# Performance work log

Measured on AMD Instinct MI355X. Metric: run time of the kernel, lower is better.

Reference implementation:

```python
import jax, jax.numpy as jnp
import numpy as np

N = 220500          # samples (5 s @ 44.1 kHz)
C = 28              # gammatone channels
L_GT = 1000         # gammatone FIR length (source default)
L_ENV = 2000        # envelope FIR length (source default)
START2POLE = 5      # Start2PoleHP -> HP applied to channels 4: (24 channels)
NGAMMA = 4          # cascaded gammatone passes
RECOMB_DB = 10.0    # Recombination_dB
EQUIV0DBSPL = 100.0 # CONFIG.equiv0dBSPL
AHR = 0.0           # CONFIG.ahr


def fir_grouped(x, h):
    """Causal per-channel FIR: y[c,n] = sum_k h[c,k] x[c,n-k]. x:[C,N], h:[C,L]."""
    L = h.shape[1]
    y = jax.lax.conv_general_dilated(
        x[None], h[:, None, ::-1], (1,), [(L - 1, 0)],
        feature_group_count=x.shape[0],
        dimension_numbers=("NCH", "OIH", "NCH"))
    return y[0]


def fir1(x, h):
    return fir_grouped(x[None, :], h[None, :])[0]


def setup_inputs() -> dict:
    key = jax.random.key(0)
    ks = jax.random.split(key, 10)
    dec_gt = jnp.exp(-jnp.arange(L_GT, dtype=jnp.float32) / 80.0)
    dec_env = jnp.exp(-jnp.arange(L_ENV, dtype=jnp.float32) / 300.0)
    x = jax.random.normal(ks[0], (N,), dtype=jnp.float32)
    gtn_imp = jax.random.normal(ks[1], (C, L_GT), dtype=jnp.float32) * 0.05 * dec_gt[None]
    hp_imp = jax.random.normal(ks[2], (C - START2POLE + 1, L_GT), dtype=jnp.float32) * 0.05 * dec_gt[None]
    chan_lpf_imp = (0.01 + 0.002 * jax.random.normal(ks[3], (C, L_ENV), dtype=jnp.float32)) * dec_env[None]
    delta256 = jnp.zeros((256,), jnp.float32).at[0].set(1.0)
    src_fwd = delta256 + 0.01 * jax.random.normal(ks[4], (256,), dtype=jnp.float32)
    src_bwd = delta256 + 0.01 * jax.random.normal(ks[5], (256,), dtype=jnp.float32)
    lpf = jnp.zeros((133,), jnp.float32).at[0].set(1.0) + 0.01 * jax.random.normal(ks[6], (133,), dtype=jnp.float32)
    expansion_ratios = 1.0 + jax.random.uniform(ks[7], (C,), dtype=jnp.float32)
    eq_loud_db = 100.0 + 10.0 * jax.random.uniform(ks[8], (C,), dtype=jnp.float32)
    delays = jax.random.randint(ks[9], (C,), 0, 200, dtype=jnp.int32)
    return {"x": x, "src_fwd": src_fwd, "src_bwd": src_bwd, "lpf": lpf,
            "gtn_imp": gtn_imp, "hp_imp": hp_imp, "chan_lpf_imp": chan_lpf_imp,
            "expansion_ratios": expansion_ratios, "eq_loud_db": eq_loud_db,
            "delays": delays}


def _cochlea(x, gtn_imp, hp_imp, chan_lpf_imp, delays, expansion_ratios, eq_loud_db, equiv_0dB_SPL):
    n = x.shape[0]
    c = gtn_imp.shape[0]
    # gammatone filterbank: NGAMMA cascaded grouped causal FIRs
    pass_n = jnp.broadcast_to(x[None, :], (c, n))
    for _ in range(NGAMMA):
        pass_n = fir_grouped(pass_n, gtn_imp)
    # per-channel delay compensation (shift left by dly, zero-fill tail)
    idx = jnp.arange(n, dtype=jnp.int32)[None, :] + delays[:, None]  # [C,N]
    gathered = jnp.take_along_axis(pass_n, jnp.minimum(idx, n - 1), axis=1)
    pass_del = jnp.where(idx < n, gathered, 0.0)
    # high-pass correction on channels Start2PoleHP-1:
    s = START2POLE - 1
    pass_del = pass_del.at[s:].set(fir_grouped(pass_del[s:], hp_imp))
    # envelope: forward-backward low-pass of rectified signal
    env_f = fir_grouped(jnp.abs(pass_del), chan_lpf_imp)
    env = fir_grouped(jnp.abs(env_f[:, ::-1]), chan_lpf_imp)[:, ::-1]
    # loudness recruitment
    envlp_max = (10.0 ** (0.05 * (eq_loud_db - equiv_0dB_SPL)))[:, None]
    env_cl = jnp.minimum(jnp.clip(env, 1e-9, None), envlp_max)
    env_norm = jnp.clip(env_cl / envlp_max, 1e-6, None)
    gain = env_norm ** (jnp.clip(expansion_ratios, -5.0, None)[:, None] - 1.0)
    gain = jnp.minimum(gain, 100.0)
    coch = pass_del * gain
    power = 10.0 ** (-0.05 * RECOMB_DB)
    return coch.sum(axis=0) * power


def reference(x, src_fwd, src_bwd, lpf, gtn_imp, hp_imp, chan_lpf_imp,
              expansion_ratios, eq_loud_db, delays):
    # level bookkeeping (as in HearingLoss.forward)
    levelreFS = 10.0 * jnp.log10(jnp.mean(x ** 2))  # noqa: F841 (calibration only)
    equiv_0dB_SPL = EQUIV0DBSPL + AHR
    # free-field -> cochlea correction
    xc = fir1(x, src_fwd)
    coch = _cochlea(xc, gtn_imp, hp_imp, chan_lpf_imp, delays,
                    expansion_ratios, eq_loud_db, equiv_0dB_SPL)
    # cochlea -> free-field correction, then 18 kHz anti-alias LPF
    out = fir1(fir1(coch, src_bwd), lpf)
    return out
```

## Files before the change

### kernel.cpp

```cpp
#include <hip/hip_runtime.h>
#include <math.h>

#define NSAMP 220500
#define NCH   28
#define HPCH  24
#define TILE  2048
#define BLOCK 256

#define LP_GT4 4032
#define LP_HP  1008
#define LP_ENV 2016
#define LP_SRC 288
#define LP_LPF 144

#define NC_GT 126
#define NC_HP 33
#define NC_EF 64
#define NC_EB 63

typedef __attribute__((ext_vector_type(4))) float f32x4;
typedef __attribute__((ext_vector_type(8))) short bf16x8;

__device__ __forceinline__ int phys9(int u) { return u + (u >> 3); }

__device__ __forceinline__ unsigned short f2bf(float x) {
    unsigned u = __float_as_uint(x);
    u += 0x7FFFu + ((u >> 16) & 1u);
    return (unsigned short)(u >> 16);
}

#define MFMA32 __builtin_amdgcn_mfma_f32_16x16x32_bf16

__global__ void prep_frag(const float* __restrict__ taps, int pitch,
                          unsigned short* __restrict__ TF, int NC,
                          int isAsc, int split, long planeStride)
{
    const int s  = blockIdx.x;
    const int ch = blockIdx.y;
    const int l  = threadIdx.x;
    const int m  = l & 15, hib = (l >> 4) * 8;
    unsigned short* dst = TF + ((size_t)ch * NC + s) * 512 + l * 8;
#pragma unroll
    for (int i = 0; i < 8; i++) {
        int kap = hib + i;
        int k = isAsc ? (32 * s + kap - m) : (32 * s + m - 1 - kap);
        float val = (k >= 0 && k < pitch) ? taps[(size_t)ch * pitch + k] : 0.f;
        unsigned short hh = f2bf(val);
        dst[i] = hh;
        if (split) {
            float fh = __uint_as_float((unsigned)hh << 16);
            dst[planeStride + i] = f2bf(val - fh);
        }
    }
}

template<int NC, bool ASC, bool SPLIT, bool ABSIN, bool DELAYED, bool GAIN>
__global__ __launch_bounds__(BLOCK)
void fir_mfma_pc(const float* __restrict__ in, long instride,
                 const unsigned short* __restrict__ TF, long planeStride,
                 float* __restrict__ out,
                 const int* __restrict__ delays, int chan0,
                 const float* __restrict__ ratios,
                 const float* __restrict__ eqloud)
{
    extern __shared__ float S[];
    unsigned short* sw = (unsigned short*)S;
    const int c  = blockIdx.y;
    const int jb = blockIdx.x * 4096;
    const float* __restrict__ xin = in + (long)c * instride;
    constexpr int E = 4112 + 32 * (NC - 1);
    const int o = ASC ? jb : (jb + 1 - 32 * (NC - 1));
    int d = 0;
    if (DELAYED) d = delays[chan0 + c];

    for (int e = threadIdx.x; e < E; e += BLOCK) {
        int p = o + e;
        float v = 0.f;
        if (DELAYED) { if (p >= 0 && p + d < NSAMP) v = xin[p + d]; }
        else         { if (p >= 0 && p < NSAMP)     v = xin[p]; }
        if (ABSIN) v = fabsf(v);
        sw[2 * phys9(e >> 1) + (e & 1)] = f2bf(v);
    }
    __syncthreads();

    const int lane = threadIdx.x & 63;
    const int w    = threadIdx.x >> 6;
    const int n    = lane & 15;
    const int hi   = lane >> 4;
    int vp = phys9(8 * n + 4 * hi + 512 * w + (ASC ? 0 : 16 * (NC - 1)));
    constexpr int DSTEP = ASC ? 18 : -18;

    const unsigned short* tp = TF + (size_t)c * NC * 512 + lane * 8;

    f32x4 ac0 = {0,0,0,0}, ac1 = {0,0,0,0}, ac2 = {0,0,0,0}, ac3 = {0,0,0,0};
    bf16x8 Ah = *(const bf16x8*)tp;
    bf16x8 Al = Ah;
    if (SPLIT) Al = *(const bf16x8*)(tp + planeStride);

#pragma unroll 1
    for (int s = 0; s < NC; ++s) {
        bf16x8 Nh = Ah, Nl = Al;
        if (s + 1 < NC) {
            Nh = *(const bf16x8*)(tp + (size_t)(s + 1) * 512);
            if (SPLIT) Nl = *(const bf16x8*)(tp + planeStride + (size_t)(s + 1) * 512);
        }
        const float* sp = S + vp;
        union U { float f[4]; bf16x8 v; };
        U b0, b1, b2, b3;
        b0.f[0]=sp[0];   b0.f[1]=sp[1];   b0.f[2]=sp[2];   b0.f[3]=sp[3];
        b1.f[0]=sp[144]; b1.f[1]=sp[145]; b1.f[2]=sp[146]; b1.f[3]=sp[147];
        b2.f[0]=sp[288]; b2.f[1]=sp[289]; b2.f[2]=sp[290]; b2.f[3]=sp[291];
        b3.f[0]=sp[432]; b3.f[1]=sp[433]; b3.f[2]=sp[434]; b3.f[3]=sp[435];
        ac0 = MFMA32(Ah, b0.v, ac0, 0, 0, 0);
        ac1 = MFMA32(Ah, b1.v, ac1, 0, 0, 0);
        ac2 = MFMA32(Ah, b2.v, ac2, 0, 0, 0);
        ac3 = MFMA32(Ah, b3.v, ac3, 0, 0, 0);
        if (SPLIT) {
            ac0 = MFMA32(Al, b0.v, ac0, 0, 0, 0);
            ac1 = MFMA32(Al, b1.v, ac1, 0, 0, 0);
            ac2 = MFMA32(Al, b2.v, ac2, 0, 0, 0);
            ac3 = MFMA32(Al, b3.v, ac3, 0, 0, 0);
        }
        Ah = Nh;
        if (SPLIT) Al = Nl;
        vp += DSTEP;
    }

    float* __restrict__ yo = out + (long)c * NSAMP;
    const int j0 = jb + 1024 * w + 16 * n + 4 * hi;

    if (!GAIN) {
        if (j0 < NSAMP)       *(f32x4*)(yo + j0)       = ac0;
        if (j0 + 256 < NSAMP) *(f32x4*)(yo + j0 + 256) = ac1;
        if (j0 + 512 < NSAMP) *(f32x4*)(yo + j0 + 512) = ac2;
        if (j0 + 768 < NSAMP) *(f32x4*)(yo + j0 + 768) = ac3;
    } else {
        const float emax = exp10f(0.05f * (eqloud[c] - 100.0f));
        const float er   = fmaxf(ratios[c], -5.0f) - 1.0f;
#define GAINST(ACC, OFS) { int j = j0 + (OFS); if (j < NSAMP) {            \
            f32x4 pv = *(f32x4*)(yo + j);                                   \
            _Pragma("unroll")                                               \
            for (int r = 0; r < 4; r++) {                                   \
                float env = ACC[r];                                         \
                float ecl = fminf(fmaxf(env, 1e-9f), emax);                 \
                float enr = fmaxf(ecl / emax, 1e-6f);                       \
                float g   = fminf(powf(enr, er), 100.0f);                   \
                pv[r] *= g;                                                 \
            }                                                               \
            *(f32x4*)(yo + j) = pv; } }
        GAINST(ac0, 0) GAINST(ac1, 256) GAINST(ac2, 512) GAINST(ac3, 768)
#undef GAINST
    }
}

static inline size_t lds_pc(int NC)
{
    int E = 4112 + 32 * (NC - 1);
    int D = (E + 1) / 2;
    return (size_t)(D + (D >> 3) + 8) * 4;
}

template<bool ASC>
__device__ __forceinline__ void group8r(const float (&LO)[8], const float (&HI)[8],
                                        float (&acc)[8], const f32x4 (&T)[2])
{
#pragma unroll
    for (int kp = 0; kp < 8; kp++) {
        const float hk = T[kp >> 2][kp & 3];
#pragma unroll
        for (int j = 0; j < 8; j++) {
            const int m = ASC ? (j + kp) : (8 + j - kp);
            const float w = (m < 8) ? LO[m] : HI[m - 8];
            acc[j] = fmaf(hk, w, acc[j]);
        }
    }
}

template<int Lpad, bool DELAYED>
__global__ __launch_bounds__(BLOCK)
void fir_blk(const float* __restrict__ in, long instride,
             const float* __restrict__ taps, int tapstride,
             float* __restrict__ out, long ostride,
             const int* __restrict__ delays, int chan0)
{
    extern __shared__ float s[];
    const int c  = blockIdx.y;
    const int n0 = blockIdx.x * TILE;
    const float* __restrict__ xin = in + (long)c * instride;
    float* __restrict__ y         = out + (long)c * ostride;
    int d = 0;
    if (DELAYED) d = delays[chan0 + c];

    constexpr int E = TILE + Lpad - 1;
    for (int i = threadIdx.x; i < E; i += BLOCK) {
        int p = n0 - (Lpad - 1) + i;
        float v = 0.f;
        if (p >= 0 && p < NSAMP) {
            int q = p + d;
            if (!DELAYED || q < NSAMP) v = xin[q];
        }
        s[phys9(i + 9)] = v;
    }
    __syncthreads();

    const int t = threadIdx.x;
    constexpr int LB = Lpad / 8;
    const int B = 9 * (t + LB);
    const f32x4* tv = (const f32x4*)(taps + (long)c * tapstride);

    float Ab[8], Bb[8], Cb[8];
    float acc[8] = {0,0,0,0,0,0,0,0};
#pragma unroll
    for (int m = 0; m < 8; m++) Ab[m] = s[B + m];
#pragma unroll
    for (int m = 0; m < 8; m++) Bb[m] = s[B + 9 + m];
    f32x4 TA[2], TB[2];
    TA[0] = tv[0]; TA[1] = tv[1];

    int Mb = B - 54;
    constexpr int NIT6 = Lpad / 48;
#pragma unroll 1
    for (int im = 0; im < NIT6; ++im) {
        const float* p = s + Mb;
#pragma unroll
        for (int m = 0; m < 8; m++) Cb[m] = p[45 + m];
        TB[0] = tv[2];  TB[1] = tv[3];
        group8r<false>(Ab, Bb, acc, TA);
#pragma unroll
        for (int m = 0; m < 8; m++) Bb[m] = p[36 + m];
        TA[0] = tv[4];  TA[1] = tv[5];
        group8r<false>(Cb, Ab, acc, TB);
#pragma unroll
        for (int m = 0; m < 8; m++) Ab[m] = p[27 + m];
        TB[0] = tv[6];  TB[1] = tv[7];
        group8r<false>(Bb, Cb, acc, TA);
#pragma unroll
        for (int m = 0; m < 8; m++) Cb[m] = p[18 + m];
        TA[0] = tv[8];  TA[1] = tv[9];
        group8r<false>(Ab, Bb, acc, TB);
#pragma unroll
        for (int m = 0; m < 8; m++) Bb[m] = p[9 + m];
        TB[0] = tv[10]; TB[1] = tv[11];
        group8r<false>(Cb, Ab, acc, TA);
#pragma unroll
        for (int m = 0; m < 8; m++) Ab[m] = p[0 + m];
        TA[0] = tv[12]; TA[1] = tv[13];
        group8r<false>(Bb, Cb, acc, TB);
        Mb -= 54;
        tv += 12;
    }

    const int nb = n0 + 8 * t;
#pragma unroll
    for (int j = 0; j < 8; j++)
        if (nb + j < NSAMP) y[nb + j] = acc[j];
}

static inline size_t lds_blk(int Lpad)
{
    int umax = TILE + Lpad + 8;
    return (size_t)(umax + (umax >> 3) + 16) * 4;
}

__global__ void conv_self(const float* __restrict__ a, int astride, int La,
                          float* __restrict__ out, int ostride, int Mlen, int Mpad)
{
    extern __shared__ float s[];
    const int c = blockIdx.y;
    const float* __restrict__ ar = a + (long)c * astride;
    for (int i = threadIdx.x; i < La; i += blockDim.x) s[i] = ar[i];
    __syncthreads();
    int m = blockIdx.x * blockDim.x + threadIdx.x;
    float acc = 0.f;
    for (int k = 0; k < La; k++) {
        int mi = m - k;
        float bv = ((unsigned)mi < (unsigned)La) ? s[mi] : 0.f;
        acc = fmaf(s[k], bv, acc);
    }
    if (m < Mpad) out[(long)c * ostride + m] = (m < Mlen) ? acc : 0.f;
}

__global__ void pad_copy(const float* __restrict__ src, int L, int sstride,
                         float* __restrict__ dst, int Lpad)
{
    int c = blockIdx.y;
    int k = blockIdx.x * blockDim.x + threadIdx.x;
    if (k < Lpad) dst[(long)c * Lpad + k] = (k < L) ? src[(long)c * sstride + k] : 0.f;
}

__global__ void delay_copy(const float* __restrict__ a, float* __restrict__ b,
                           const int* __restrict__ delays)
{
    int c = blockIdx.y;
    int n = blockIdx.x * blockDim.x + threadIdx.x;
    if (n < NSAMP) {
        int q = n + delays[c];
        b[(long)c * NSAMP + n] = (q < NSAMP) ? a[(long)c * NSAMP + q] : 0.f;
    }
}

__global__ void reduce_coch(const float* __restrict__ b, float* __restrict__ coch)
{
    int n = blockIdx.x * blockDim.x + threadIdx.x;
    if (n < NSAMP) {
        float sum = 0.f;
        for (int c = 0; c < NCH; c++) sum += b[(long)c * NSAMP + n];
        coch[n] = sum * 0.31622776601683794f;
    }
}

extern "C" void kernel_launch(void* const* d_in, const int* in_sizes, int n_in,
                              void* d_out, int out_size, void* d_ws, size_t ws_size,
                              hipStream_t stream)
{
    const float* x       = (const float*)d_in[0];
    const float* src_fwd = (const float*)d_in[1];
    const float* src_bwd = (const float*)d_in[2];
    const float* lpf     = (const float*)d_in[3];
    const float* gtn     = (const float*)d_in[4];
    const float* hp      = (const float*)d_in[5];
    const float* clpf    = (const float*)d_in[6];
    const float* ratios  = (const float*)d_in[7];
    const float* eqloud  = (const float*)d_in[8];
    const int*   delays  = (const int*)d_in[9];
    float* out = (float*)d_out;

    float* ws   = (float*)d_ws;
    const size_t CNs = (size_t)NCH * NSAMP;
    float* bufA  = ws;
    float* bufB  = bufA + CNs;
    float* xc    = bufB + CNs;
    float* coch  = xc + NSAMP;
    float* t1    = coch + NSAMP;
    float* h2    = t1 + NSAMP;
    float* h4    = h2 + (size_t)NCH * 2000;
    float* hpP   = h4 + (size_t)NCH * LP_GT4;
    float* clpfP = hpP + (size_t)HPCH * LP_HP;
    float* sfP   = clpfP + (size_t)NCH * LP_ENV;
    float* sbP   = sfP + LP_SRC;
    float* lpP   = sbP + LP_SRC;

    unsigned short* TFgt = (unsigned short*)(lpP + LP_LPF);
    const long gtPlane = (long)NCH * NC_GT * 512;
    unsigned short* TFhp = TFgt + 2 * gtPlane;
    unsigned short* TFef = TFhp + (size_t)HPCH * NC_HP * 512;
    unsigned short* TFeb = TFef + (size_t)NCH * NC_EF * 512;

    dim3 blk(BLOCK);
    const int NT  = (NSAMP + TILE - 1) / TILE;
    const int NB4 = (NSAMP + 4095) / 4096;

    conv_self<<<dim3(8, NCH), blk, 1000 * 4, stream>>>(
        gtn, 1000, 1000, h2, 2000, 1999, 1999);
    conv_self<<<dim3((LP_GT4 + BLOCK - 1) / BLOCK, NCH), blk, 1999 * 4, stream>>>(
        h2, 2000, 1999, h4, LP_GT4, 3997, LP_GT4);
    pad_copy<<<dim3(4, HPCH), blk, 0, stream>>>(hp, 1000, 1000, hpP, LP_HP);
    pad_copy<<<dim3(8, NCH), blk, 0, stream>>>(clpf, 2000, 2000, clpfP, LP_ENV);
    pad_copy<<<dim3(2, 1), blk, 0, stream>>>(src_fwd, 256, 256, sfP, LP_SRC);
    pad_copy<<<dim3(2, 1), blk, 0, stream>>>(src_bwd, 256, 256, sbP, LP_SRC);
    pad_copy<<<dim3(1, 1), blk, 0, stream>>>(lpf, 133, 133, lpP, LP_LPF);

    prep_frag<<<dim3(NC_GT, NCH), dim3(64), 0, stream>>>(
        h4, LP_GT4, TFgt, NC_GT, 0, 1, gtPlane);
    prep_frag<<<dim3(NC_HP, HPCH), dim3(64), 0, stream>>>(
        hpP, LP_HP, TFhp, NC_HP, 0, 0, 0);
    prep_frag<<<dim3(NC_EF, NCH), dim3(64), 0, stream>>>(
        clpfP, LP_ENV, TFef, NC_EF, 0, 0, 0);
    prep_frag<<<dim3(NC_EB, NCH), dim3(64), 0, stream>>>(
        clpfP, LP_ENV, TFeb, NC_EB, 1, 0, 0);

    fir_blk<LP_SRC, false><<<dim3(NT, 1), blk, lds_blk(LP_SRC), stream>>>(
        x, 0, sfP, LP_SRC, xc, 0, nullptr, 0);

    fir_mfma_pc<NC_GT, false, true, false, false, false>
        <<<dim3(NB4, NCH), blk, lds_pc(NC_GT), stream>>>(
        xc, 0, TFgt, gtPlane, bufA, nullptr, 0, nullptr, nullptr);

    delay_copy<<<dim3((NSAMP + BLOCK - 1) / BLOCK, 4), blk, 0, stream>>>(
        bufA, bufB, delays);

    fir_mfma_pc<NC_HP, false, false, false, true, false>
        <<<dim3(NB4, HPCH), blk, lds_pc(NC_HP), stream>>>(
        bufA + 4 * (size_t)NSAMP, NSAMP, TFhp, 0, bufB + 4 * (size_t)NSAMP,
        delays, 4, nullptr, nullptr);

    fir_mfma_pc<NC_EF, false, false, true, false, false>
        <<<dim3(NB4, NCH), blk, lds_pc(NC_EF), stream>>>(
        bufB, NSAMP, TFef, 0, bufA, nullptr, 0, nullptr, nullptr);

    fir_mfma_pc<NC_EB, true, false, true, false, true>
        <<<dim3(NB4, NCH), blk, lds_pc(NC_EB), stream>>>(
        bufA, NSAMP, TFeb, 0, bufB, nullptr, 0, ratios, eqloud);

    reduce_coch<<<dim3((NSAMP + BLOCK - 1) / BLOCK), blk, 0, stream>>>(bufB, coch);

    fir_blk<LP_SRC, false><<<dim3(NT, 1), blk, lds_blk(LP_SRC), stream>>>(
        coch, 0, sbP, LP_SRC, t1, 0, nullptr, 0);
    fir_blk<LP_LPF, false><<<dim3(NT, 1), blk, lds_blk(LP_LPF), stream>>>(
        t1, 0, lpP, LP_LPF, out, 0, nullptr, 0);
}
```

Before: 500.9 us.

## Fold source FIRs into gammatone/tail filters and switch to 32x32 MFMA kernels

The forward source FIR is pre-convolved into the quadrupled gammatone impulse response, and the backward source FIR is pre-convolved with the anti-alias LPF, which removes two full-length signal passes and their intermediate buffers. The gammatone pass now computes four channels per block so each LDS tile of the input is reused across channels. The HP and envelope FIRs move to a new kernel built on 32x32x16 bf16 MFMA with a different LDS padding scheme. The trade-offs are longer combined filters (more MFMA steps) and a larger accumulator register footprint per wave.

```diff
diff --git a/kernel.cpp b/kernel.cpp
--- a/kernel.cpp
+++ b/kernel.cpp
@@ -8,18 +8,21 @@
 #define BLOCK 256
 
 #define LP_GT4 4032
+#define L_H4F  4252
+#define LP_H4F 4288
 #define LP_HP  1008
 #define LP_ENV 2016
-#define LP_SRC 288
-#define LP_LPF 144
-
-#define NC_GT 126
-#define NC_HP 33
-#define NC_EF 64
-#define NC_EB 63
-
-typedef __attribute__((ext_vector_type(4))) float f32x4;
-typedef __attribute__((ext_vector_type(8))) short bf16x8;
+#define L_TB   388
+#define LP_TB  432
+
+#define NC_GT 134
+#define NC_HP 65
+#define NC_EF 128
+#define NC_EB 128
+
+typedef __attribute__((ext_vector_type(4)))  float f32x4;
+typedef __attribute__((ext_vector_type(16))) float f32x16;
+typedef __attribute__((ext_vector_type(8)))  short bf16x8;
 
 __device__ __forceinline__ int phys9(int u) { return u + (u >> 3); }
 
@@ -29,7 +32,8 @@
     return (unsigned short)(u >> 16);
 }
 
-#define MFMA32 __builtin_amdgcn_mfma_f32_16x16x32_bf16
+#define MFMA16 __builtin_amdgcn_mfma_f32_16x16x32_bf16
+#define MFMA32 __builtin_amdgcn_mfma_f32_32x32x16_bf16
 
 __global__ void prep_frag(const float* __restrict__ taps, int pitch,
                           unsigned short* __restrict__ TF, int NC,
@@ -54,110 +58,209 @@
     }
 }
 
-template<int NC, bool ASC, bool SPLIT, bool ABSIN, bool DELAYED, bool GAIN>
+__global__ void prep_frag32(const float* __restrict__ taps, int pitch,
+                            unsigned short* __restrict__ TF, int NC, int isAsc)
+{
+    const int s  = blockIdx.x;
+    const int ch = blockIdx.y;
+    const int l  = threadIdx.x;
+    const int m  = l & 31, kb = (l >> 5) * 8;
+    unsigned short* dst = TF + ((size_t)ch * NC + s) * 512 + l * 8;
+#pragma unroll
+    for (int i = 0; i < 8; i++) {
+        int kap = kb + i;
+        int k = isAsc ? (16 * s + kap - m) : (16 * s + m - 17 - kap);
+        float val = (k >= 0 && k < pitch) ? taps[(size_t)ch * pitch + k] : 0.f;
+        dst[i] = f2bf(val);
+    }
+}
+
 __global__ __launch_bounds__(BLOCK)
-void fir_mfma_pc(const float* __restrict__ in, long instride,
-                 const unsigned short* __restrict__ TF, long planeStride,
-                 float* __restrict__ out,
-                 const int* __restrict__ delays, int chan0,
-                 const float* __restrict__ ratios,
-                 const float* __restrict__ eqloud)
+void gt4_mfma4(const float* __restrict__ x, const unsigned short* __restrict__ TF,
+               long plane, float* __restrict__ out)
 {
     extern __shared__ float S[];
-    unsigned short* sw = (unsigned short*)S;
-    const int c  = blockIdx.y;
-    const int jb = blockIdx.x * 4096;
-    const float* __restrict__ xin = in + (long)c * instride;
-    constexpr int E = 4112 + 32 * (NC - 1);
-    const int o = ASC ? jb : (jb + 1 - 32 * (NC - 1));
-    int d = 0;
-    if (DELAYED) d = delays[chan0 + c];
-
-    for (int e = threadIdx.x; e < E; e += BLOCK) {
-        int p = o + e;
-        float v = 0.f;
-        if (DELAYED) { if (p >= 0 && p + d < NSAMP) v = xin[p + d]; }
-        else         { if (p >= 0 && p < NSAMP)     v = xin[p]; }
-        if (ABSIN) v = fabsf(v);
-        sw[2 * phys9(e >> 1) + (e & 1)] = f2bf(v);
+    unsigned* S32 = (unsigned*)S;
+    const int jb = blockIdx.x * 2048;
+    const int c0 = blockIdx.y * 4;
+    const int o  = jb - 4255;
+    const int DW = 3160;
+
+    for (int v = threadIdx.x; v < DW; v += BLOCK) {
+        int p0 = o + 2 * v, p1 = p0 + 1;
+        float a = (p0 >= 0 && p0 < NSAMP) ? x[p0] : 0.f;
+        float b = (p1 >= 0 && p1 < NSAMP) ? x[p1] : 0.f;
+        S32[v + (v >> 4)] = (unsigned)f2bf(a) | ((unsigned)f2bf(b) << 16);
     }
     __syncthreads();
 
     const int lane = threadIdx.x & 63;
     const int w    = threadIdx.x >> 6;
     const int n    = lane & 15;
-    const int hi   = lane >> 4;
-    int vp = phys9(8 * n + 4 * hi + 512 * w + (ASC ? 0 : 16 * (NC - 1)));
-    constexpr int DSTEP = ASC ? 18 : -18;
+    const int hib  = lane >> 4;
+    int v0 = 256 * w + 8 * n + 4 * hib + 16 * (NC_GT - 1);
+    int vp = v0 + (v0 >> 4);
+
+    const unsigned short* t0  = TF + lane * 8;
+    const unsigned short* tc0 = t0 + (size_t)(c0 + 0) * NC_GT * 512;
+    const unsigned short* tc1 = t0 + (size_t)(c0 + 1) * NC_GT * 512;
+    const unsigned short* tc2 = t0 + (size_t)(c0 + 2) * NC_GT * 512;
+    const unsigned short* tc3 = t0 + (size_t)(c0 + 3) * NC_GT * 512;
+
+    f32x4 a00={0,0,0,0}, a01={0,0,0,0}, a10={0,0,0,0}, a11={0,0,0,0};
+    f32x4 a20={0,0,0,0}, a21={0,0,0,0}, a30={0,0,0,0}, a31={0,0,0,0};
+
+    bf16x8 h0 = *(const bf16x8*)tc0, h1 = *(const bf16x8*)tc1;
+    bf16x8 h2 = *(const bf16x8*)tc2, h3 = *(const bf16x8*)tc3;
+    bf16x8 l0 = *(const bf16x8*)(tc0 + plane), l1 = *(const bf16x8*)(tc1 + plane);
+    bf16x8 l2 = *(const bf16x8*)(tc2 + plane), l3 = *(const bf16x8*)(tc3 + plane);
+
+#pragma unroll 1
+    for (int s = 0; s < NC_GT; ++s) {
+        int sn = (s + 1 < NC_GT) ? s + 1 : s;
+        size_t off = (size_t)sn * 512;
+        bf16x8 nh0 = *(const bf16x8*)(tc0 + off);
+        bf16x8 nh1 = *(const bf16x8*)(tc1 + off);
+        bf16x8 nh2 = *(const bf16x8*)(tc2 + off);
+        bf16x8 nh3 = *(const bf16x8*)(tc3 + off);
+        bf16x8 nl0 = *(const bf16x8*)(tc0 + plane + off);
+        bf16x8 nl1 = *(const bf16x8*)(tc1 + plane + off);
+        bf16x8 nl2 = *(const bf16x8*)(tc2 + plane + off);
+        bf16x8 nl3 = *(const bf16x8*)(tc3 + plane + off);
+
+        const float* sp = S + vp;
+        union U { float f[4]; bf16x8 v; } b0, b1;
+        b0.f[0]=sp[0];   b0.f[1]=sp[1];   b0.f[2]=sp[2];   b0.f[3]=sp[3];
+        b1.f[0]=sp[136]; b1.f[1]=sp[137]; b1.f[2]=sp[138]; b1.f[3]=sp[139];
+
+        a00 = MFMA16(h0, b0.v, a00,0,0,0);  a00 = MFMA16(l0, b0.v, a00,0,0,0);
+        a10 = MFMA16(h1, b0.v, a10,0,0,0);  a10 = MFMA16(l1, b0.v, a10,0,0,0);
+        a20 = MFMA16(h2, b0.v, a20,0,0,0);  a20 = MFMA16(l2, b0.v, a20,0,0,0);
+        a30 = MFMA16(h3, b0.v, a30,0,0,0);  a30 = MFMA16(l3, b0.v, a30,0,0,0);
+        a01 = MFMA16(h0, b1.v, a01,0,0,0);  a01 = MFMA16(l0, b1.v, a01,0,0,0);
+        a11 = MFMA16(h1, b1.v, a11,0,0,0);  a11 = MFMA16(l1, b1.v, a11,0,0,0);
+        a21 = MFMA16(h2, b1.v, a21,0,0,0);  a21 = MFMA16(l2, b1.v, a21,0,0,0);
+        a31 = MFMA16(h3, b1.v, a31,0,0,0);  a31 = MFMA16(l3, b1.v, a31,0,0,0);
+
+        h0=nh0; h1=nh1; h2=nh2; h3=nh3;
+        l0=nl0; l1=nl1; l2=nl2; l3=nl3;
+        vp -= 17;
+    }
+
+    const int j0 = jb + 512 * w + 16 * n + 4 * hib;
+    float* y0 = out + (size_t)(c0 + 0) * NSAMP;
+    float* y1 = out + (size_t)(c0 + 1) * NSAMP;
+    float* y2 = out + (size_t)(c0 + 2) * NSAMP;
+    float* y3 = out + (size_t)(c0 + 3) * NSAMP;
+    if (j0 < NSAMP) {
+        *(f32x4*)(y0 + j0) = a00; *(f32x4*)(y1 + j0) = a10;
+        *(f32x4*)(y2 + j0) = a20; *(f32x4*)(y3 + j0) = a30;
+    }
+    if (j0 + 256 < NSAMP) {
+        *(f32x4*)(y0 + j0 + 256) = a01; *(f32x4*)(y1 + j0 + 256) = a11;
+        *(f32x4*)(y2 + j0 + 256) = a21; *(f32x4*)(y3 + j0 + 256) = a31;
+    }
+}
+
+template<int NC, bool ASC, bool ABSIN, bool DELAYED, bool GAIN>
+__global__ __launch_bounds__(BLOCK)
+void fir32(const float* __restrict__ in, long instride,
+           const unsigned short* __restrict__ TF,
+           float* __restrict__ out,
+           const int* __restrict__ delays, int chan0,
+           const float* __restrict__ ratios, const float* __restrict__ eqloud)
+{
+    extern __shared__ float S[];
+    unsigned* S32 = (unsigned*)S;
+    const int c  = blockIdx.y;
+    const int jb = blockIdx.x * 4096;
+    const float* __restrict__ xin = in + (size_t)c * instride;
+    const int o = ASC ? jb : (jb + 17 - 16 * (NC - 1));
+    int d = 0;
+    if (DELAYED) d = delays[chan0 + c];
+
+    const int DW = 2040 + 8 * (NC - 1);
+    for (int v = threadIdx.x; v < DW; v += BLOCK) {
+        int p0 = o + 2 * v, p1 = p0 + 1;
+        float a = 0.f, b = 0.f;
+        if (DELAYED) {
+            if (p0 >= 0 && p0 + d < NSAMP) a = xin[p0 + d];
+            if (p1 >= 0 && p1 + d < NSAMP) b = xin[p1 + d];
+        } else {
+            if (p0 >= 0 && p0 < NSAMP) a = xin[p0];
+            if (p1 >= 0 && p1 < NSAMP) b = xin[p1];
+        }
+        if (ABSIN) { a = fabsf(a); b = fabsf(b); }
+        S32[v + (v >> 4)] = (unsigned)f2bf(a) | ((unsigned)f2bf(b) << 16);
+    }
+    __syncthreads();
+
+    const int lane = threadIdx.x & 63;
+    const int w    = threadIdx.x >> 6;
+    const int n    = lane & 31;
+    const int h5   = lane >> 5;
+    int v = 512 * w + 16 * n + 4 * h5 + (ASC ? 0 : 8 * (NC - 1));
 
     const unsigned short* tp = TF + (size_t)c * NC * 512 + lane * 8;
 
-    f32x4 ac0 = {0,0,0,0}, ac1 = {0,0,0,0}, ac2 = {0,0,0,0}, ac3 = {0,0,0,0};
-    bf16x8 Ah = *(const bf16x8*)tp;
-    bf16x8 Al = Ah;
-    if (SPLIT) Al = *(const bf16x8*)(tp + planeStride);
+    f32x16 acc;
+#pragma unroll
+    for (int i = 0; i < 16; ++i) acc[i] = 0.f;
+    bf16x8 A = *(const bf16x8*)tp;
 
 #pragma unroll 1
     for (int s = 0; s < NC; ++s) {
-        bf16x8 Nh = Ah, Nl = Al;
-        if (s + 1 < NC) {
-            Nh = *(const bf16x8*)(tp + (size_t)(s + 1) * 512);
-            if (SPLIT) Nl = *(const bf16x8*)(tp + planeStride + (size_t)(s + 1) * 512);
+        int sn = (s + 1 < NC) ? s + 1 : s;
+        bf16x8 An = *(const bf16x8*)(tp + (size_t)sn * 512);
+        int vp = v + (v >> 4);
+        const float* sp = S + vp;
+        union U { float f[4]; bf16x8 v; } B;
+        B.f[0] = sp[0]; B.f[1] = sp[1]; B.f[2] = sp[2]; B.f[3] = sp[3];
+        acc = MFMA32(A, B.v, acc, 0, 0, 0);
+        A = An;
+        v += ASC ? 8 : -8;
+    }
+
+    float* __restrict__ yo = out + (size_t)c * NSAMP;
+    const int jbase = jb + 1024 * w + 32 * n + 4 * h5;
+    if (!GAIN) {
+#pragma unroll
+        for (int g = 0; g < 4; ++g) {
+            int j0 = jbase + 8 * g;
+            if (j0 < NSAMP) {
+                f32x4 st;
+                st[0] = acc[4*g+0]; st[1] = acc[4*g+1];
+                st[2] = acc[4*g+2]; st[3] = acc[4*g+3];
+                *(f32x4*)(yo + j0) = st;
+            }
         }
-        const float* sp = S + vp;
-        union U { float f[4]; bf16x8 v; };
-        U b0, b1, b2, b3;
-        b0.f[0]=sp[0];   b0.f[1]=sp[1];   b0.f[2]=sp[2];   b0.f[3]=sp[3];
-        b1.f[0]=sp[144]; b1.f[1]=sp[145]; b1.f[2]=sp[146]; b1.f[3]=sp[147];
-        b2.f[0]=sp[288]; b2.f[1]=sp[289]; b2.f[2]=sp[290]; b2.f[3]=sp[291];
-        b3.f[0]=sp[432]; b3.f[1]=sp[433]; b3.f[2]=sp[434]; b3.f[3]=sp[435];
-        ac0 = MFMA32(Ah, b0.v, ac0, 0, 0, 0);
-        ac1 = MFMA32(Ah, b1.v, ac1, 0, 0, 0);
-        ac2 = MFMA32(Ah, b2.v, ac2, 0, 0, 0);
-        ac3 = MFMA32(Ah, b3.v, ac3, 0, 0, 0);
-        if (SPLIT) {
-            ac0 = MFMA32(Al, b0.v, ac0, 0, 0, 0);
-            ac1 = MFMA32(Al, b1.v, ac1, 0, 0, 0);
-            ac2 = MFMA32(Al, b2.v, ac2, 0, 0, 0);
-            ac3 = MFMA32(Al, b3.v, ac3, 0, 0, 0);
-        }
-        Ah = Nh;
-        if (SPLIT) Al = Nl;
-        vp += DSTEP;
-    }
-
-    float* __restrict__ yo = out + (long)c * NSAMP;
-    const int j0 = jb + 1024 * w + 16 * n + 4 * hi;
-
-    if (!GAIN) {
-        if (j0 < NSAMP)       *(f32x4*)(yo + j0)       = ac0;
-        if (j0 + 256 < NSAMP) *(f32x4*)(yo + j0 + 256) = ac1;
-        if (j0 + 512 < NSAMP) *(f32x4*)(yo + j0 + 512) = ac2;
-        if (j0 + 768 < NSAMP) *(f32x4*)(yo + j0 + 768) = ac3;
     } else {
         const float emax = exp10f(0.05f * (eqloud[c] - 100.0f));
         const float er   = fmaxf(ratios[c], -5.0f) - 1.0f;
-#define GAINST(ACC, OFS) { int j = j0 + (OFS); if (j < NSAMP) {            \
-            f32x4 pv = *(f32x4*)(yo + j);                                   \
-            _Pragma("unroll")                                               \
-            for (int r = 0; r < 4; r++) {                                   \
-                float env = ACC[r];                                         \
-                float ecl = fminf(fmaxf(env, 1e-9f), emax);                 \
-                float enr = fmaxf(ecl / emax, 1e-6f);                       \
-                float g   = fminf(powf(enr, er), 100.0f);                   \
-                pv[r] *= g;                                                 \
-            }                                                               \
-            *(f32x4*)(yo + j) = pv; } }
-        GAINST(ac0, 0) GAINST(ac1, 256) GAINST(ac2, 512) GAINST(ac3, 768)
-#undef GAINST
-    }
-}
-
-static inline size_t lds_pc(int NC)
-{
-    int E = 4112 + 32 * (NC - 1);
-    int D = (E + 1) / 2;
-    return (size_t)(D + (D >> 3) + 8) * 4;
+#pragma unroll
+        for (int g = 0; g < 4; ++g) {
+            int j0 = jbase + 8 * g;
+            if (j0 < NSAMP) {
+                f32x4 pv = *(f32x4*)(yo + j0);
+#pragma unroll
+                for (int q = 0; q < 4; ++q) {
+                    float env = acc[4*g+q];
+                    float ecl = fminf(fmaxf(env, 1e-9f), emax);
+                    float enr = fmaxf(ecl / emax, 1e-6f);
+                    float gg  = fminf(powf(enr, er), 100.0f);
+                    pv[q] *= gg;
+                }
+                *(f32x4*)(yo + j0) = pv;
+            }
+        }
+    }
+}
+
+static inline size_t lds_gt4() { return (size_t)(3160 + (3160 >> 4) + 8) * 4; }
+static inline size_t lds32(int NC)
+{
+    int DW = 2040 + 8 * (NC - 1);
+    return (size_t)(DW + (DW >> 4) + 8) * 4;
 }
 
 template<bool ASC>
@@ -280,6 +383,24 @@
     if (m < Mpad) out[(long)c * ostride + m] = (m < Mlen) ? acc : 0.f;
 }
 
+__global__ void conv_pair(const float* __restrict__ a, int astride, int La,
+                          const float* __restrict__ b, int Lb,
+                          float* __restrict__ out, int ostride, int Mlen, int Mpad)
+{
+    extern __shared__ float s[];
+    const int c = blockIdx.y;
+    for (int i = threadIdx.x; i < Lb; i += blockDim.x) s[i] = b[i];
+    __syncthreads();
+    int m = blockIdx.x * blockDim.x + threadIdx.x;
+    float acc = 0.f;
+    for (int k = 0; k < Lb; k++) {
+        int mi = m - k;
+        float av = ((unsigned)mi < (unsigned)La) ? a[(size_t)c * astride + mi] : 0.f;
+        acc = fmaf(s[k], av, acc);
+    }
+    if (m < Mpad) out[(size_t)c * ostride + m] = (m < Mlen) ? acc : 0.f;
+}
+
 __global__ void pad_copy(const float* __restrict__ src, int L, int sstride,
                          float* __restrict__ dst, int Lpad)
 {
@@ -325,77 +446,66 @@
     const int*   delays  = (const int*)d_in[9];
     float* out = (float*)d_out;
 
-    float* ws   = (float*)d_ws;
+    float* ws = (float*)d_ws;
     const size_t CNs = (size_t)NCH * NSAMP;
     float* bufA  = ws;
     float* bufB  = bufA + CNs;
-    float* xc    = bufB + CNs;
-    float* coch  = xc + NSAMP;
-    float* t1    = coch + NSAMP;
-    float* h2    = t1 + NSAMP;
+    float* coch  = bufB + CNs;
+    float* h2    = coch + NSAMP;
     float* h4    = h2 + (size_t)NCH * 2000;
-    float* hpP   = h4 + (size_t)NCH * LP_GT4;
+    float* h4f   = h4 + (size_t)NCH * LP_GT4;
+    float* hpP   = h4f + (size_t)NCH * LP_H4F;
     float* clpfP = hpP + (size_t)HPCH * LP_HP;
-    float* sfP   = clpfP + (size_t)NCH * LP_ENV;
-    float* sbP   = sfP + LP_SRC;
-    float* lpP   = sbP + LP_SRC;
-
-    unsigned short* TFgt = (unsigned short*)(lpP + LP_LPF);
+    float* tb    = clpfP + (size_t)NCH * LP_ENV;
+
+    unsigned short* TFgt = (unsigned short*)(tb + LP_TB);
     const long gtPlane = (long)NCH * NC_GT * 512;
     unsigned short* TFhp = TFgt + 2 * gtPlane;
     unsigned short* TFef = TFhp + (size_t)HPCH * NC_HP * 512;
     unsigned short* TFeb = TFef + (size_t)NCH * NC_EF * 512;
 
     dim3 blk(BLOCK);
-    const int NT  = (NSAMP + TILE - 1) / TILE;
-    const int NB4 = (NSAMP + 4095) / 4096;
 
     conv_self<<<dim3(8, NCH), blk, 1000 * 4, stream>>>(
         gtn, 1000, 1000, h2, 2000, 1999, 1999);
-    conv_self<<<dim3((LP_GT4 + BLOCK - 1) / BLOCK, NCH), blk, 1999 * 4, stream>>>(
+    conv_self<<<dim3(16, NCH), blk, 1999 * 4, stream>>>(
         h2, 2000, 1999, h4, LP_GT4, 3997, LP_GT4);
+    conv_pair<<<dim3((LP_H4F + BLOCK - 1) / BLOCK, NCH), blk, 256 * 4, stream>>>(
+        h4, LP_GT4, 3997, src_fwd, 256, h4f, LP_H4F, L_H4F, LP_H4F);
+    conv_pair<<<dim3(2, 1), blk, 133 * 4, stream>>>(
+        src_bwd, 0, 256, lpf, 133, tb, LP_TB, L_TB, LP_TB);
     pad_copy<<<dim3(4, HPCH), blk, 0, stream>>>(hp, 1000, 1000, hpP, LP_HP);
     pad_copy<<<dim3(8, NCH), blk, 0, stream>>>(clpf, 2000, 2000, clpfP, LP_ENV);
-    pad_copy<<<dim3(2, 1), blk, 0, stream>>>(src_fwd, 256, 256, sfP, LP_SRC);
-    pad_copy<<<dim3(2, 1), blk, 0, stream>>>(src_bwd, 256, 256, sbP, LP_SRC);
-    pad_copy<<<dim3(1, 1), blk, 0, stream>>>(lpf, 133, 133, lpP, LP_LPF);
 
     prep_frag<<<dim3(NC_GT, NCH), dim3(64), 0, stream>>>(
-        h4, LP_GT4, TFgt, NC_GT, 0, 1, gtPlane);
-    prep_frag<<<dim3(NC_HP, HPCH), dim3(64), 0, stream>>>(
-        hpP, LP_HP, TFhp, NC_HP, 0, 0, 0);
-    prep_frag<<<dim3(NC_EF, NCH), dim3(64), 0, stream>>>(
-        clpfP, LP_ENV, TFef, NC_EF, 0, 0, 0);
-    prep_frag<<<dim3(NC_EB, NCH), dim3(64), 0, stream>>>(
-        clpfP, LP_ENV, TFeb, NC_EB, 1, 0, 0);
-
-    fir_blk<LP_SRC, false><<<dim3(NT, 1), blk, lds_blk(LP_SRC), stream>>>(
-        x, 0, sfP, LP_SRC, xc, 0, nullptr, 0);
-
-    fir_mfma_pc<NC_GT, false, true, false, false, false>
-        <<<dim3(NB4, NCH), blk, lds_pc(NC_GT), stream>>>(
-        xc, 0, TFgt, gtPlane, bufA, nullptr, 0, nullptr, nullptr);
+        h4f, LP_H4F, TFgt, NC_GT, 0, 1, gtPlane);
+    prep_frag32<<<dim3(NC_HP, HPCH), dim3(64), 0, stream>>>(
+        hpP, LP_HP, TFhp, NC_HP, 0);
+    prep_frag32<<<dim3(NC_EF, NCH), dim3(64), 0, stream>>>(
+        clpfP, LP_ENV, TFef, NC_EF, 0);
+    prep_frag32<<<dim3(NC_EB, NCH), dim3(64), 0, stream>>>(
+        clpfP, LP_ENV, TFeb, NC_EB, 1);
+
+    gt4_mfma4<<<dim3(108, 7), blk, lds_gt4(), stream>>>(x, TFgt, gtPlane, bufA);
 
     delay_copy<<<dim3((NSAMP + BLOCK - 1) / BLOCK, 4), blk, 0, stream>>>(
         bufA, bufB, delays);
 
-    fir_mfma_pc<NC_HP, false, false, false, true, false>
-        <<<dim3(NB4, HPCH), blk, lds_pc(NC_HP), stream>>>(
-        bufA + 4 * (size_t)NSAMP, NSAMP, TFhp, 0, bufB + 4 * (size_t)NSAMP,
+    fir32<NC_HP, false, false, true, false>
+        <<<dim3(54, HPCH), blk, lds32(NC_HP), stream>>>(
+        bufA + 4 * (size_t)NSAMP, NSAMP, TFhp, bufB + 4 * (size_t)NSAMP,
         delays, 4, nullptr, nullptr);
 
-    fir_mfma_pc<NC_EF, false, false, true, false, false>
-        <<<dim3(NB4, NCH), blk, lds_pc(NC_EF), stream>>>(
-        bufB, NSAMP, TFef, 0, bufA, nullptr, 0, nullptr, nullptr);
-
-    fir_mfma_pc<NC_EB, true, false, true, false, true>
-        <<<dim3(NB4, NCH), blk, lds_pc(NC_EB), stream>>>(
-        bufA, NSAMP, TFeb, 0, bufB, nullptr, 0, ratios, eqloud);
+    fir32<NC_EF, false, true, false, false>
+        <<<dim3(54, NCH), blk, lds32(NC_EF), stream>>>(
+        bufB, NSAMP, TFef, bufA, nullptr, 0, nullptr, nullptr);
+
+    fir32<NC_EB, true, true, false, true>
+        <<<dim3(54, NCH), blk, lds32(NC_EB), stream>>>(
+        bufA, NSAMP, TFeb, bufB, nullptr, 0, ratios, eqloud);
 
     reduce_coch<<<dim3((NSAMP + BLOCK - 1) / BLOCK), blk, 0, stream>>>(bufB, coch);
 
-    fir_blk<LP_SRC, false><<<dim3(NT, 1), blk, lds_blk(LP_SRC), stream>>>(
-        coch, 0, sbP, LP_SRC, t1, 0, nullptr, 0);
-    fir_blk<LP_LPF, false><<<dim3(NT, 1), blk, lds_blk(LP_LPF), stream>>>(
-        t1, 0, lpP, LP_LPF, out, 0, nullptr, 0);
-}
+    fir_blk<LP_TB, false><<<dim3(108, 1), blk, lds_blk(LP_TB), stream>>>(
+        coch, 0, tb, LP_TB, out, 0, nullptr, 0);
+}
```

Measured after the change: 496.5 us. Within noise of the previous version (-0.9%).
